# Kernel optimization log

Hardware: AMD Instinct MI355X
Metric: run time of the kernel (lower is better)

The kernel has to match this reference:

```python
import jax, jax.numpy as jnp
import numpy as np

B, C, T, H, W = 2, 256, 16, 32, 32
NH = 8
GROUPS = 32
EPS = 1e-6


def setup_inputs() -> dict:
    key = jax.random.key(0)
    ks = jax.random.split(key, 10)
    r = lambda k, shape: jax.random.normal(k, shape, dtype=jnp.float32) * 0.02
    return dict(
        x=jax.random.normal(ks[0], (B, C, T, H, W), dtype=jnp.float32),
        gn_gamma=jnp.ones((C,), jnp.float32),
        gn_beta=jnp.zeros((C,), jnp.float32),
        wq_s=r(ks[1], (C, C)), bq_s=jnp.zeros((C,), jnp.float32),
        wk_s=r(ks[2], (C, C)), bk_s=jnp.zeros((C,), jnp.float32),
        wv_s=r(ks[3], (C, C)), bv_s=jnp.zeros((C,), jnp.float32),
        wo_s=r(ks[4], (C, C)), bo_s=jnp.zeros((C,), jnp.float32),
        wq_t=r(ks[5], (C, C)),
        wk_t=r(ks[6], (C, C)),
        wv_t=r(ks[7], (C, C)),
        wf_t=r(ks[8], (C, C)), bf_t=jnp.zeros((C,), jnp.float32),
    )


def group_norm(x, gamma, beta):
    # x: (N, C, H, W), GroupNorm(32, eps=1e-6, affine)
    n, c, h, w = x.shape
    xg = x.reshape(n, GROUPS, c // GROUPS, h, w)
    mu = xg.mean(axis=(2, 3, 4), keepdims=True)
    var = xg.var(axis=(2, 3, 4), keepdims=True)
    xg = (xg - mu) * jax.lax.rsqrt(var + EPS)
    return xg.reshape(n, c, h, w) * gamma[None, :, None, None] + beta[None, :, None, None]


def spatial_attention(x, gn_gamma, gn_beta, wq, bq, wk, bk, wv, bv, wo, bo):
    # ldm SpatialSelfAttention: norm -> 1x1 conv q/k/v -> full HW self-attn -> 1x1 proj -> residual
    n, c, h, w = x.shape
    hf = group_norm(x, gn_gamma, gn_beta).reshape(n, c, h * w)  # (N, C, HW)
    q = jnp.einsum('oc,bcn->bno', wq, hf) + bq                  # (N, HW, C)
    k = jnp.einsum('oc,bcn->bon', wk, hf) + bk[None, :, None]   # (N, C, HW)
    v = jnp.einsum('oc,bcn->bon', wv, hf) + bv[None, :, None]   # (N, C, HW)
    attn = jax.nn.softmax(jnp.einsum('bic,bcj->bij', q, k) * (c ** -0.5), axis=-1)  # (N, HW, HW)
    out = jnp.einsum('bcj,bij->bci', v, attn)                   # (N, C, HW)
    out = jnp.einsum('oc,bcn->bon', wo, out) + bo[None, :, None]
    return x + out.reshape(n, c, h, w)


def axial_temporal_attention(x, wq, wk, wv, wf, bf):
    # x: (B, T, H, W, C); VideoGPT MultiHeadAttention with AxialAttention over T (axial_dim=-4)
    b, t, h, w, c = x.shape
    dk = c // NH

    def heads(y):  # (B,T,H,W,C) -> (B,H,W,NH,T,dk)
        return jnp.transpose(y.reshape(b, t, h, w, NH, dk), (0, 2, 3, 4, 1, 5))

    q = heads(x @ wq)
    k = heads(x @ wk)
    v = heads(x @ wv)
    scores = jnp.einsum('bhwntd,bhwnsd->bhwnts', q, k) / jnp.sqrt(jnp.float32(dk))
    attn = jax.nn.softmax(scores, axis=-1)
    out = jnp.einsum('bhwnts,bhwnsd->bhwntd', attn, v)          # (B,H,W,NH,T,dk)
    out = jnp.transpose(out, (0, 4, 1, 2, 3, 5)).reshape(b, t, h, w, c)
    return out @ wf + bf


def reference(x, gn_gamma, gn_beta, wq_s, bq_s, wk_s, bk_s, wv_s, bv_s, wo_s, bo_s,
              wq_t, wk_t, wv_t, wf_t, bf_t):
    b, c, t, h, w = x.shape
    # spatial branch: torch does a raw reshape (B,C,T,H,W)->(B*T,C,H,W); replicate exactly
    s = spatial_attention(x.reshape(b * t, c, h, w), gn_gamma, gn_beta,
                          wq_s, bq_s, wk_s, bk_s, wv_s, bv_s, wo_s, bo_s)
    s = s.reshape(b, c, t, h, w)
    # temporal branch: channels-last, axial attention over T
    xt = jnp.moveaxis(x, 1, -1)                                 # (B,T,H,W,C)
    tt = axial_temporal_attention(xt, wq_t, wk_t, wv_t, wf_t, bf_t)
    return s + jnp.moveaxis(tt, -1, 1)
```

## Files before the change

### kernel.cpp

```cpp
#include <hip/hip_runtime.h>
#include <stdint.h>

typedef uint16_t u16;
typedef __attribute__((ext_vector_type(8))) short s8v;
typedef __attribute__((ext_vector_type(4))) float f32x4;
typedef __attribute__((ext_vector_type(4))) unsigned short us4;

__device__ __forceinline__ float bf2f(u16 u) {
  union { uint32_t i; float f; } x; x.i = ((uint32_t)u) << 16; return x.f;
}
__device__ __forceinline__ u16 f2bf(float f) {
  union { float f; uint32_t i; } x; x.f = f;
  uint32_t r = (x.i + 0x7FFFu + ((x.i >> 16) & 1u)) >> 16;
  return (u16)r;
}
__device__ __forceinline__ void gl2lds16(const u16* g, u16* l) {
  __builtin_amdgcn_global_load_lds(
      (const __attribute__((address_space(1))) uint32_t*)g,
      (__attribute__((address_space(3))) uint32_t*)l, 16, 0, 0);
}

__global__ __launch_bounds__(256) void gn_stats_kernel(const float* __restrict__ x,
                                                       float2* __restrict__ stats) {
  const int tid = threadIdx.x;
  const float* p = x + (long)blockIdx.x * 8192;
  float s = 0.f, s2 = 0.f;
#pragma unroll
  for (int it = 0; it < 8; ++it) {
    float4 v = *(const float4*)(p + it * 1024 + tid * 4);
    s  += v.x + v.y + v.z + v.w;
    s2 += v.x * v.x + v.y * v.y + v.z * v.z + v.w * v.w;
  }
#pragma unroll
  for (int off = 32; off >= 1; off >>= 1) {
    s  += __shfl_down(s, off);
    s2 += __shfl_down(s2, off);
  }
  __shared__ float ps[4], ps2[4];
  const int wv = tid >> 6, lane = tid & 63;
  if (lane == 0) { ps[wv] = s; ps2[wv] = s2; }
  __syncthreads();
  if (tid == 0) {
    float S1 = ps[0] + ps[1] + ps[2] + ps[3];
    float S2 = ps2[0] + ps2[1] + ps2[2] + ps2[3];
    float mean = S1 * (1.f / 8192.f);
    float var = S2 * (1.f / 8192.f) - mean * mean;
    stats[blockIdx.x] = make_float2(mean, rsqrtf(var + 1e-6f));
  }
}

__global__ __launch_bounds__(256) void wprep_kernel(
    const float* __restrict__ s0, const float* __restrict__ s1,
    const float* __restrict__ s2, const float* __restrict__ s3,
    const float* __restrict__ s4, const float* __restrict__ s5,
    const float* __restrict__ s6, const float* __restrict__ s7,
    u16* __restrict__ wbf) {
  const int mat = blockIdx.x, rb = blockIdx.y;
  const float* src = mat==0?s0:mat==1?s1:mat==2?s2:mat==3?s3:mat==4?s4:mat==5?s5:mat==6?s6:s7;
  u16* dst = wbf + mat * 65536 + rb * 16384;
  const int tid = threadIdx.x;
  if (mat < 4) {
    const float* sb = src + rb * 16384;
#pragma unroll
    for (int it = 0; it < 16; ++it) {
      int idx = it * 256 + tid;
      float4 v = *(const float4*)(sb + idx * 4);
      us4 o; o[0]=f2bf(v.x); o[1]=f2bf(v.y); o[2]=f2bf(v.z); o[3]=f2bf(v.w);
      *(us4*)(dst + idx * 4) = o;
    }
  } else {
    __shared__ u16 tl[64][264];
#pragma unroll
    for (int it = 0; it < 16; ++it) {
      int idx = it * 256 + tid;
      int c = idx >> 4, o4 = idx & 15;
      float4 v = *(const float4*)(src + c * 256 + rb * 64 + o4 * 4);
      tl[o4*4+0][c] = f2bf(v.x);
      tl[o4*4+1][c] = f2bf(v.y);
      tl[o4*4+2][c] = f2bf(v.z);
      tl[o4*4+3][c] = f2bf(v.w);
    }
    __syncthreads();
#pragma unroll
    for (int it = 0; it < 16; ++it) {
      int idx = it * 256 + tid;
      int o = idx >> 6, c4 = idx & 63;
      us4 u;
#pragma unroll
      for (int j = 0; j < 4; ++j) u[j] = tl[o][c4*4+j];
      *(us4*)(dst + o * 256 + c4 * 4) = u;
    }
  }
}

__global__ __launch_bounds__(512) void qkv_s_kernel(
    const float* __restrict__ x, const float2* __restrict__ stats,
    const float* __restrict__ gamma, const float* __restrict__ beta,
    const u16* __restrict__ wbf,
    const float* __restrict__ bq, const float* __restrict__ bk, const float* __restrict__ bv,
    u16* __restrict__ qb, u16* __restrict__ kb, u16* __restrict__ vb) {
  __shared__ float gas[256], bes[256];
  __shared__ u16 ALDS[128 * 256];
  __shared__ u16 WLDS[2][64 * 256];
  const int bid = blockIdx.x;
  const int n = bid >> 3, pt = bid & 7;
  const int p0 = pt * 128;
  const int tid = threadIdx.x, w = tid >> 6, lane = tid & 63;
  const int lhi = lane >> 4, llo = lane & 15;
  const long nbase = (long)n * 262144;

  if (tid < 256) {
    float2 st = stats[n * 32 + (tid >> 3)];
    float ga = gamma[tid] * st.y;
    gas[tid] = ga;
    bes[tid] = beta[tid] - st.x * ga;
  }
  __syncthreads();

  const float* xb = x + nbase + p0;
#pragma unroll
  for (int it = 0; it < 16; ++it) {
    int idx = it * 512 + tid;
    int p = idx & 127, c4 = idx >> 7;
    us4 o;
#pragma unroll
    for (int j = 0; j < 4; ++j) {
      int c = c4 * 4 + j;
      float v = xb[(long)c * 1024 + p];
      o[j] = f2bf(v * gas[c] + bes[c]);
    }
    int ch = c4 >> 1;
    *(us4*)&ALDS[p * 256 + ((ch ^ (p & 7)) << 3) + ((c4 & 1) << 2)] = o;
  }
  __syncthreads();

  const int arow = w * 16 + llo;
  s8v qa[8];
#pragma unroll
  for (int kk = 0; kk < 8; ++kk)
    qa[kk] = *(const s8v*)&ALDS[arow * 256 + (((kk * 4 + lhi) ^ (arow & 7)) << 3)];

  auto stageW = [&](int t, int bu) {
    const u16* wsrc = wbf + (t >> 2) * 65536 + (long)(t & 3) * 16384;
#pragma unroll
    for (int ii = 0; ii < 4; ++ii) {
      int i0 = (w * 4 + ii) * 64;
      int g = i0 + lane;
      int row = g >> 5, ch = g & 31;
      gl2lds16(wsrc + row * 256 + ((ch ^ (row & 7)) << 3), &WLDS[bu][i0 * 8]);
    }
  };

  stageW(0, 0);
  __syncthreads();

  u16* vtl = ALDS;
  for (int t = 0; t < 12; ++t) {
    const int cur = t & 1;
    if (t < 11) stageW(t + 1, cur ^ 1);
    f32x4 acc[4] = {};
#pragma unroll
    for (int kk = 0; kk < 8; ++kk)
#pragma unroll
      for (int nf = 0; nf < 4; ++nf) {
        int row = nf * 16 + llo;
        s8v bfr = *(const s8v*)&WLDS[cur][row * 256 + (((kk * 4 + lhi) ^ (row & 7)) << 3)];
        acc[nf] = __builtin_amdgcn_mfma_f32_16x16x32_bf16(qa[kk], bfr, acc[nf], 0, 0, 0);
      }
    const int o0 = (t & 3) * 64;
    if (t < 8) {
      u16* dstb = (t < 4) ? qb : kb;
      const float* bias = (t < 4) ? bq : bk;
#pragma unroll
      for (int nf = 0; nf < 4; ++nf) {
        int o = o0 + nf * 16 + llo;
        float b_ = bias[o];
#pragma unroll
        for (int r = 0; r < 4; ++r)
          dstb[nbase + (long)(p0 + w * 16 + lhi * 4 + r) * 256 + o] = f2bf(acc[nf][r] + b_);
      }
    } else {
#pragma unroll
      for (int nf = 0; nf < 4; ++nf) {
        int o = nf * 16 + llo;
        float b_ = bv[o0 + o];
#pragma unroll
        for (int r = 0; r < 4; ++r)
          vtl[o * 136 + w * 16 + lhi * 4 + r] = f2bf(acc[nf][r] + b_);
      }
      __syncthreads();
#pragma unroll
      for (int ii = 0; ii < 4; ++ii) {
        int i = ii * 512 + tid;
        int o = i >> 5, p4 = (i & 31) * 4;
        us4 u;
#pragma unroll
        for (int j = 0; j < 4; ++j) u[j] = vtl[o * 136 + p4 + j];
        *(us4*)(vb + nbase + (long)(o0 + o) * 1024 + p0 + p4) = u;
      }
    }
    __syncthreads();
  }
}

__global__ __launch_bounds__(512, 2) void flash_kernel(const u16* __restrict__ qb,
                                                       const u16* __restrict__ kb,
                                                       const u16* __restrict__ vb,
                                                       u16* __restrict__ attb) {
  const int wg = blockIdx.x;
  const int swz = (wg & 7) * 32 + (wg >> 3);
  const int n = swz >> 3, qt = swz & 7;
  const int tid = threadIdx.x, wid = tid >> 6, lane = tid & 63;
  const int lhi = lane >> 4, llo = lane & 15;
  const long nbase = (long)n * 262144;

  __shared__ u16 Kb[2][64 * 256];
  __shared__ u16 Vb[2][256 * 64];
  __shared__ u16 ps[128][72];

  const u16* qrow = qb + nbase + (long)(qt * 128 + wid * 16 + llo) * 256;
  s8v qa[8];
#pragma unroll
  for (int kk = 0; kk < 8; ++kk) qa[kk] = *(const s8v*)(qrow + kk * 32 + lhi * 8);

  f32x4 oacc[16] = {};
  float m_[4], l_[4];
#pragma unroll
  for (int r = 0; r < 4; ++r) { m_[r] = -3.4e38f; l_[r] = 0.f; }

  const int l5 = lane >> 5, c16 = lane & 31, l3 = lane >> 3, ch8 = lane & 7;

  auto stageKV = [&](int jt2, int b) {
    const u16* kbase = kb + nbase + (long)jt2 * 64 * 256;
    const u16* vbase = vb + nbase + (long)jt2 * 64;
#pragma unroll
    for (int ii = 0; ii < 4; ++ii) {
      int i = wid * 4 + ii;
      int r = i * 2 + l5;
      gl2lds16(kbase + (long)r * 256 + ((c16 ^ (r & 7)) * 8), &Kb[b][i * 512]);
    }
#pragma unroll
    for (int ii = 0; ii < 4; ++ii) {
      int i = wid * 4 + ii;
      int c = i * 8 + l3;
      gl2lds16(vbase + (long)c * 1024 + ((ch8 ^ (c & 7)) * 8), &Vb[b][i * 512]);
    }
  };

  stageKV(0, 0);
  __syncthreads();

  for (int jt = 0; jt < 16; ++jt) {
    const int cur = jt & 1;
    if (jt < 15) stageKV(jt + 1, cur ^ 1);

    f32x4 sacc[4] = {};
#pragma unroll
    for (int jf = 0; jf < 4; ++jf) {
      const int row = jf * 16 + llo;
      const u16* kr = &Kb[cur][row * 256];
#pragma unroll
      for (int kk = 0; kk < 8; ++kk) {
        const int chunk = (kk * 4 + lhi) ^ (row & 7);
        s8v b = *(const s8v*)(kr + chunk * 8);
        sacc[jf] = __builtin_amdgcn_mfma_f32_16x16x32_bf16(qa[kk], b, sacc[jf], 0, 0, 0);
      }
    }
#pragma unroll
    for (int jf = 0; jf < 4; ++jf)
#pragma unroll
      for (int r = 0; r < 4; ++r) sacc[jf][r] *= 0.0625f;
    float sc[4];
#pragma unroll
    for (int r = 0; r < 4; ++r) {
      float mx = fmaxf(fmaxf(sacc[0][r], sacc[1][r]), fmaxf(sacc[2][r], sacc[3][r]));
      mx = fmaxf(mx, __shfl_xor(mx, 1));
      mx = fmaxf(mx, __shfl_xor(mx, 2));
      mx = fmaxf(mx, __shfl_xor(mx, 4));
      mx = fmaxf(mx, __shfl_xor(mx, 8));
      float nm = fmaxf(m_[r], mx);
      sc[r] = __expf(m_[r] - nm);
      m_[r] = nm;
    }
    float rs[4] = {0.f, 0.f, 0.f, 0.f};
#pragma unroll
    for (int jf = 0; jf < 4; ++jf)
#pragma unroll
      for (int r = 0; r < 4; ++r) {
        float p = __expf(sacc[jf][r] - m_[r]);
        rs[r] += p;
        ps[wid * 16 + lhi * 4 + r][jf * 16 + llo] = f2bf(p);
      }
#pragma unroll
    for (int r = 0; r < 4; ++r) {
      rs[r] += __shfl_xor(rs[r], 1);
      rs[r] += __shfl_xor(rs[r], 2);
      rs[r] += __shfl_xor(rs[r], 4);
      rs[r] += __shfl_xor(rs[r], 8);
      l_[r] = l_[r] * sc[r] + rs[r];
    }
#pragma unroll
    for (int cf = 0; cf < 16; ++cf)
#pragma unroll
      for (int r = 0; r < 4; ++r) oacc[cf][r] *= sc[r];
    s8v pa[2];
#pragma unroll
    for (int kk = 0; kk < 2; ++kk)
      pa[kk] = *(const s8v*)&ps[wid * 16 + llo][kk * 32 + lhi * 8];
#pragma unroll
    for (int cf = 0; cf < 16; ++cf) {
      const int c = cf * 16 + llo;
      const u16* vr = &Vb[cur][c * 64];
#pragma unroll
      for (int kk = 0; kk < 2; ++kk) {
        const int chunk = (kk * 4 + lhi) ^ (c & 7);
        s8v b = *(const s8v*)(vr + chunk * 8);
        oacc[cf] = __builtin_amdgcn_mfma_f32_16x16x32_bf16(pa[kk], b, oacc[cf], 0, 0, 0);
      }
    }
    __syncthreads();
  }
  u16* obase = attb + nbase + (long)(qt * 128 + wid * 16) * 256;
#pragma unroll
  for (int r = 0; r < 4; ++r) {
    float inv = 1.f / l_[r];
#pragma unroll
    for (int cf = 0; cf < 16; ++cf)
      obase[(lhi * 4 + r) * 256 + cf * 16 + llo] = f2bf(oacc[cf][r] * inv);
  }
}

__global__ __launch_bounds__(512) void qkv_t_kernel(
    const float* __restrict__ x, const u16* __restrict__ wbf,
    u16* __restrict__ qt, u16* __restrict__ kt, u16* __restrict__ vt) {
  __shared__ u16 ALDS[128 * 256];
  __shared__ u16 WLDS[2][64 * 256];
  const int bid = blockIdx.x;
  const int b = bid >> 7, st = bid & 127;
  const int s0 = st * 128;
  const int tid = threadIdx.x, w = tid >> 6, lane = tid & 63;
  const int lhi = lane >> 4, llo = lane & 15;
  const long bbase = (long)b * 4194304;

  const float* xb = x + bbase + s0;
#pragma unroll
  for (int it = 0; it < 16; ++it) {
    int idx = it * 512 + tid;
    int p = idx & 127, c4 = idx >> 7;
    us4 o;
#pragma unroll
    for (int j = 0; j < 4; ++j)
      o[j] = f2bf(xb[(long)(c4 * 4 + j) * 16384 + p]);
    int ch = c4 >> 1;
    *(us4*)&ALDS[p * 256 + ((ch ^ (p & 7)) << 3) + ((c4 & 1) << 2)] = o;
  }
  __syncthreads();
  const int arow = w * 16 + llo;
  s8v qa[8];
#pragma unroll
  for (int kk = 0; kk < 8; ++kk)
    qa[kk] = *(const s8v*)&ALDS[arow * 256 + (((kk * 4 + lhi) ^ (arow & 7)) << 3)];

  auto stageW = [&](int t, int bu) {
    const u16* wsrc = wbf + (4 + (t >> 2)) * 65536 + (long)(t & 3) * 16384;
#pragma unroll
    for (int ii = 0; ii < 4; ++ii) {
      int i0 = (w * 4 + ii) * 64;
      int g = i0 + lane;
      int row = g >> 5, ch = g & 31;
      gl2lds16(wsrc + row * 256 + ((ch ^ (row & 7)) << 3), &WLDS[bu][i0 * 8]);
    }
  };
  stageW(0, 0);
  __syncthreads();
  for (int t = 0; t < 12; ++t) {
    const int cur = t & 1;
    if (t < 11) stageW(t + 1, cur ^ 1);
    f32x4 acc[4] = {};
#pragma unroll
    for (int kk = 0; kk < 8; ++kk)
#pragma unroll
      for (int nf = 0; nf < 4; ++nf) {
        int row = nf * 16 + llo;
        s8v bb = *(const s8v*)&WLDS[cur][row * 256 + (((kk * 4 + lhi) ^ (row & 7)) << 3)];
        acc[nf] = __builtin_amdgcn_mfma_f32_16x16x32_bf16(qa[kk], bb, acc[nf], 0, 0, 0);
      }
    u16* dstb = (t < 4) ? qt : (t < 8) ? kt : vt;
    const int o0 = (t & 3) * 64;
#pragma unroll
    for (int nf = 0; nf < 4; ++nf) {
      int o = o0 + nf * 16 + llo;
#pragma unroll
      for (int r = 0; r < 4; ++r)
        dstb[bbase + (long)(s0 + w * 16 + lhi * 4 + r) * 256 + o] = f2bf(acc[nf][r]);
    }
    __syncthreads();
  }
}

__global__ __launch_bounds__(256) void tattn_kernel(const u16* __restrict__ qt,
                                                    const u16* __restrict__ kt,
                                                    const u16* __restrict__ vt,
                                                    u16* __restrict__ ot) {
  const int bi = blockIdx.x >> 10, hw = blockIdx.x & 1023;
  const long base = (long)bi * 4194304 + (long)hw * 256;
  __shared__ float qs[16][260], ks[16][260], vs[16][260];
  __shared__ u16 os[16][256];
  const int tid = threadIdx.x;
#pragma unroll
  for (int it = 0; it < 4; ++it) {
    int idx = it * 256 + tid;
    int t = idx >> 6, cv = idx & 63;
    long g = base + (long)t * 262144 + cv * 4;
    us4 a = *(const us4*)(qt + g);
    us4 b = *(const us4*)(kt + g);
    us4 c = *(const us4*)(vt + g);
#pragma unroll
    for (int j = 0; j < 4; ++j) {
      qs[t][cv * 4 + j] = bf2f(a[j]);
      ks[t][cv * 4 + j] = bf2f(b[j]);
      vs[t][cv * 4 + j] = bf2f(c[j]);
    }
  }
  __syncthreads();
  if (tid < 128) {
    const int h = tid >> 4, t = tid & 15;
    const int c0 = h * 32;
    float sc[16];
    float mx = -3.4e38f;
#pragma unroll
    for (int t2 = 0; t2 < 16; ++t2) {
      float d = 0.f;
#pragma unroll
      for (int dd = 0; dd < 32; ++dd) d += qs[t][c0 + dd] * ks[t2][c0 + dd];
      sc[t2] = d * 0.17677669529663687f;
      mx = fmaxf(mx, sc[t2]);
    }
    float sum = 0.f;
#pragma unroll
    for (int t2 = 0; t2 < 16; ++t2) { sc[t2] = __expf(sc[t2] - mx); sum += sc[t2]; }
    float inv = 1.f / sum;
#pragma unroll
    for (int dd = 0; dd < 32; ++dd) {
      float o = 0.f;
#pragma unroll
      for (int t2 = 0; t2 < 16; ++t2) o += sc[t2] * vs[t2][c0 + dd];
      os[t][c0 + dd] = f2bf(o * inv);
    }
  }
  __syncthreads();
#pragma unroll
  for (int it = 0; it < 4; ++it) {
    int idx = it * 256 + tid;
    int t = idx >> 6, cv = idx & 63;
    us4 o4;
#pragma unroll
    for (int j = 0; j < 4; ++j) o4[j] = os[t][cv * 4 + j];
    *(us4*)(ot + base + (long)t * 262144 + cv * 4) = o4;
  }
}

__global__ __launch_bounds__(512) void tfinal_kernel(
    const u16* __restrict__ ott, const u16* __restrict__ wbf,
    u16* __restrict__ tmpT) {
  __shared__ u16 ALDS[128 * 256];
  __shared__ u16 WLDS[2][64 * 256];
  const int bid = blockIdx.x;
  const int b = bid >> 7, st = bid & 127;
  const int s0 = st * 128;
  const int tid = threadIdx.x, w = tid >> 6, lane = tid & 63;
  const int lhi = lane >> 4, llo = lane & 15;
  const long bbase = (long)b * 4194304;

  const u16* otS = ott + bbase + (long)s0 * 256;
#pragma unroll
  for (int ii = 0; ii < 8; ++ii) {
    int i0 = (w * 8 + ii) * 64;
    int g = i0 + lane;
    int row = g >> 5, ch = g & 31;
    gl2lds16(otS + row * 256 + ((ch ^ (row & 7)) << 3), &ALDS[i0 * 8]);
  }
  __syncthreads();
  const int arow = w * 16 + llo;
  s8v qa[8];
#pragma unroll
  for (int kk = 0; kk < 8; ++kk)
    qa[kk] = *(const s8v*)&ALDS[arow * 256 + (((kk * 4 + lhi) ^ (arow & 7)) << 3)];

  auto stageW = [&](int t, int bu) {
    const u16* wsrc = wbf + 7 * 65536 + (long)t * 16384;
#pragma unroll
    for (int ii = 0; ii < 4; ++ii) {
      int i0 = (w * 4 + ii) * 64;
      int g = i0 + lane;
      int row = g >> 5, ch = g & 31;
      gl2lds16(wsrc + row * 256 + ((ch ^ (row & 7)) << 3), &WLDS[bu][i0 * 8]);
    }
  };
  stageW(0, 0);
  __syncthreads();
  u16* vtl = ALDS;
  for (int t = 0; t < 4; ++t) {
    const int cur = t & 1;
    if (t < 3) stageW(t + 1, cur ^ 1);
    f32x4 acc[4] = {};
#pragma unroll
    for (int kk = 0; kk < 8; ++kk)
#pragma unroll
      for (int nf = 0; nf < 4; ++nf) {
        int row = nf * 16 + llo;
        s8v bb = *(const s8v*)&WLDS[cur][row * 256 + (((kk * 4 + lhi) ^ (row & 7)) << 3)];
        acc[nf] = __builtin_amdgcn_mfma_f32_16x16x32_bf16(qa[kk], bb, acc[nf], 0, 0, 0);
      }
#pragma unroll
    for (int nf = 0; nf < 4; ++nf) {
      int o = nf * 16 + llo;
#pragma unroll
      for (int r = 0; r < 4; ++r)
        vtl[o * 136 + w * 16 + lhi * 4 + r] = f2bf(acc[nf][r]);
    }
    __syncthreads();
    const int o0 = t * 64;
#pragma unroll
    for (int ii = 0; ii < 4; ++ii) {
      int i = ii * 512 + tid;
      int o = i >> 5, p4 = (i & 31) * 4;
      us4 uu;
#pragma unroll
      for (int j = 0; j < 4; ++j) uu[j] = vtl[o * 136 + p4 + j];
      *(us4*)(tmpT + bbase + (long)(o0 + o) * 16384 + s0 + p4) = uu;
    }
    __syncthreads();
  }
}

__global__ __launch_bounds__(256) void outproj_kernel(
    const float* __restrict__ x, const u16* __restrict__ attb,
    const u16* __restrict__ tmpT, const u16* __restrict__ wbf,
    const float* __restrict__ bo, const float* __restrict__ bf,
    float* __restrict__ out) {
  __shared__ u16 attL[64 * 256];
  const int u = blockIdx.x;
  const int wkx = (u & 7) * 256 + (u >> 3);
  const int otile = wkx & 3, pt = (wkx >> 2) & 15, n = wkx >> 6;
  const int b = n >> 4;
  const int o0 = otile * 64, p0 = pt * 64;
  const int tid = threadIdx.x, w = tid >> 6, lane = tid & 63;
  const int lhi = lane >> 4, llo = lane & 15;
  const long nbase = (long)n * 262144;

  const u16* attS = attb + nbase + (long)p0 * 256;
#pragma unroll
  for (int ii = 0; ii < 8; ++ii) {
    int i0 = (w * 8 + ii) * 64;
    int g = i0 + lane;
    int row = g >> 5, ch = g & 31;
    gl2lds16(attS + row * 256 + ((ch ^ (row & 7)) << 3), &attL[i0 * 8]);
  }
  const u16* woR = wbf + 3 * 65536 + (long)(o0 + w * 16 + llo) * 256;
  s8v woa[8];
#pragma unroll
  for (int kk = 0; kk < 8; ++kk)
    woa[kk] = *(const s8v*)(woR + kk * 32 + lhi * 8);
  __syncthreads();
  f32x4 acc[4] = {};
#pragma unroll
  for (int kk = 0; kk < 8; ++kk)
#pragma unroll
    for (int nf = 0; nf < 4; ++nf) {
      int row = nf * 16 + llo;
      s8v b1 = *(const s8v*)&attL[row * 256 + (((kk * 4 + lhi) ^ (row & 7)) << 3)];
      acc[nf] = __builtin_amdgcn_mfma_f32_16x16x32_bf16(woa[kk], b1, acc[nf], 0, 0, 0);
    }
#pragma unroll
  for (int r = 0; r < 4; ++r) {
    int cp = o0 + w * 16 + lhi * 4 + r;
    int co = ((n & 15) << 4) + (cp >> 4);
    int tt = cp & 15;
    float bias = bo[cp] + bf[co];
    const u16* tr = tmpT + (long)b * 4194304 + (long)co * 16384 + tt * 1024 + p0;
    const float* xr = x + nbase + (long)cp * 1024 + p0;
    float* orow = out + nbase + (long)cp * 1024 + p0;
#pragma unroll
    for (int nf = 0; nf < 4; ++nf) {
      int p = nf * 16 + llo;
      orow[p] = acc[nf][r] + bias + xr[p] + bf2f(tr[p]);
    }
  }
}

extern "C" void kernel_launch(void* const* d_in, const int* in_sizes, int n_in,
                              void* d_out, int out_size, void* d_ws, size_t ws_size,
                              hipStream_t stream) {
  const float* x     = (const float*)d_in[0];
  const float* gam   = (const float*)d_in[1];
  const float* bet   = (const float*)d_in[2];
  const float* wq_s  = (const float*)d_in[3];
  const float* bq_s  = (const float*)d_in[4];
  const float* wk_s  = (const float*)d_in[5];
  const float* bk_s  = (const float*)d_in[6];
  const float* wv_s  = (const float*)d_in[7];
  const float* bv_s  = (const float*)d_in[8];
  const float* wo_s  = (const float*)d_in[9];
  const float* bo_s  = (const float*)d_in[10];
  const float* wq_t  = (const float*)d_in[11];
  const float* wk_t  = (const float*)d_in[12];
  const float* wv_t  = (const float*)d_in[13];
  const float* wf_t  = (const float*)d_in[14];
  const float* bf_t  = (const float*)d_in[15];
  float* out = (float*)d_out;

  u16* qb   = (u16*)d_ws;
  u16* kb   = qb + 8388608;
  u16* vb   = kb + 8388608;
  u16* attb = vb + 8388608;
  u16* ottb = attb + 8388608;
  u16* wbf  = ottb + 8388608;
  float2* stats = (float2*)(wbf + 524288);
  u16* qt = qb; u16* kt = kb; u16* vt = vb;
  u16* tmpT = qb;

  gn_stats_kernel<<<1024, 256, 0, stream>>>(x, stats);
  wprep_kernel<<<dim3(8, 4), 256, 0, stream>>>(wq_s, wk_s, wv_s, wo_s,
                                               wq_t, wk_t, wv_t, wf_t, wbf);
  qkv_s_kernel<<<256, 512, 0, stream>>>(x, stats, gam, bet, wbf,
                                        bq_s, bk_s, bv_s, qb, kb, vb);
  flash_kernel<<<256, 512, 0, stream>>>(qb, kb, vb, attb);
  qkv_t_kernel<<<256, 512, 0, stream>>>(x, wbf, qt, kt, vt);
  tattn_kernel<<<2048, 256, 0, stream>>>(qt, kt, vt, ottb);
  tfinal_kernel<<<256, 512, 0, stream>>>(ottb, wbf, tmpT);
  outproj_kernel<<<2048, 256, 0, stream>>>(x, attb, tmpT, wbf, bo_s, bf_t, out);
}
```

Before: 207.2 us.

## Rewrite spatial flash attention with 32x32 MFMA and register-resident P

Measured after the change: 203.0 us. 2.0% less time.

```diff
diff --git a/kernel.cpp b/kernel.cpp
--- a/kernel.cpp
+++ b/kernel.cpp
@@ -4,7 +4,9 @@
 typedef uint16_t u16;
 typedef __attribute__((ext_vector_type(8))) short s8v;
 typedef __attribute__((ext_vector_type(4))) float f32x4;
+typedef __attribute__((ext_vector_type(16))) float f32x16;
 typedef __attribute__((ext_vector_type(4))) unsigned short us4;
+typedef __attribute__((ext_vector_type(4))) unsigned int u32x4;
 
 __device__ __forceinline__ float bf2f(u16 u) {
   union { uint32_t i; float f; } x; x.i = ((uint32_t)u) << 16; return x.f;
@@ -13,6 +15,11 @@
   union { float f; uint32_t i; } x; x.f = f;
   uint32_t r = (x.i + 0x7FFFu + ((x.i >> 16) & 1u)) >> 16;
   return (u16)r;
+}
+__device__ __forceinline__ uint32_t cvtpk(float a, float b) {
+  uint32_t r;
+  asm("v_cvt_pk_bf16_f32 %0, %1, %2" : "=v"(r) : "v"(a), "v"(b));
+  return r;
 }
 __device__ __forceinline__ void gl2lds16(const u16* g, u16* l) {
   __builtin_amdgcn_global_load_lds(
@@ -203,47 +210,44 @@
   }
 }
 
-__global__ __launch_bounds__(512, 2) void flash_kernel(const u16* __restrict__ qb,
+__global__ __launch_bounds__(256, 1) void flash_kernel(const u16* __restrict__ qb,
                                                        const u16* __restrict__ kb,
                                                        const u16* __restrict__ vb,
                                                        u16* __restrict__ attb) {
   const int wg = blockIdx.x;
   const int swz = (wg & 7) * 32 + (wg >> 3);
   const int n = swz >> 3, qt = swz & 7;
-  const int tid = threadIdx.x, wid = tid >> 6, lane = tid & 63;
-  const int lhi = lane >> 4, llo = lane & 15;
+  const int tid = threadIdx.x, w = tid >> 6, lane = tid & 63;
+  const int q5 = lane & 31, h = lane >> 5;
   const long nbase = (long)n * 262144;
 
   __shared__ u16 Kb[2][64 * 256];
   __shared__ u16 Vb[2][256 * 64];
-  __shared__ u16 ps[128][72];
-
-  const u16* qrow = qb + nbase + (long)(qt * 128 + wid * 16 + llo) * 256;
-  s8v qa[8];
-#pragma unroll
-  for (int kk = 0; kk < 8; ++kk) qa[kk] = *(const s8v*)(qrow + kk * 32 + lhi * 8);
-
-  f32x4 oacc[16] = {};
-  float m_[4], l_[4];
-#pragma unroll
-  for (int r = 0; r < 4; ++r) { m_[r] = -3.4e38f; l_[r] = 0.f; }
-
-  const int l5 = lane >> 5, c16 = lane & 31, l3 = lane >> 3, ch8 = lane & 7;
+
+  const int qrow = qt * 128 + w * 32 + q5;
+  const u16* qr = qb + nbase + (long)qrow * 256 + h * 8;
+  s8v qa[16];
+#pragma unroll
+  for (int kk = 0; kk < 16; ++kk) qa[kk] = *(const s8v*)(qr + kk * 16);
+
+  f32x16 oaccT[8] = {};
+  float m_ = -3.4e38f, l_ = 0.f;
+  constexpr float CEXP = 0.09016844f;
 
   auto stageKV = [&](int jt2, int b) {
     const u16* kbase = kb + nbase + (long)jt2 * 64 * 256;
     const u16* vbase = vb + nbase + (long)jt2 * 64;
 #pragma unroll
-    for (int ii = 0; ii < 4; ++ii) {
-      int i = wid * 4 + ii;
-      int r = i * 2 + l5;
-      gl2lds16(kbase + (long)r * 256 + ((c16 ^ (r & 7)) * 8), &Kb[b][i * 512]);
-    }
-#pragma unroll
-    for (int ii = 0; ii < 4; ++ii) {
-      int i = wid * 4 + ii;
-      int c = i * 8 + l3;
-      gl2lds16(vbase + (long)c * 1024 + ((ch8 ^ (c & 7)) * 8), &Vb[b][i * 512]);
+    for (int ii = 0; ii < 8; ++ii) {
+      int slot = ii * 256 + tid;
+      int row = slot >> 5, ch = slot & 31;
+      gl2lds16(kbase + (long)row * 256 + ((ch ^ (row & 7)) << 3), &Kb[b][slot * 8]);
+    }
+#pragma unroll
+    for (int ii = 0; ii < 8; ++ii) {
+      int slot = ii * 256 + tid;
+      int c = slot >> 3, ch = slot & 7;
+      gl2lds16(vbase + (long)c * 1024 + ((ch ^ (c & 7)) << 3), &Vb[b][slot * 8]);
     }
   };
 
@@ -254,79 +258,96 @@
     const int cur = jt & 1;
     if (jt < 15) stageKV(jt + 1, cur ^ 1);
 
-    f32x4 sacc[4] = {};
-#pragma unroll
-    for (int jf = 0; jf < 4; ++jf) {
-      const int row = jf * 16 + llo;
-      const u16* kr = &Kb[cur][row * 256];
-#pragma unroll
-      for (int kk = 0; kk < 8; ++kk) {
-        const int chunk = (kk * 4 + lhi) ^ (row & 7);
-        s8v b = *(const s8v*)(kr + chunk * 8);
-        sacc[jf] = __builtin_amdgcn_mfma_f32_16x16x32_bf16(qa[kk], b, sacc[jf], 0, 0, 0);
-      }
-    }
-#pragma unroll
-    for (int jf = 0; jf < 4; ++jf)
-#pragma unroll
-      for (int r = 0; r < 4; ++r) sacc[jf][r] *= 0.0625f;
-    float sc[4];
-#pragma unroll
-    for (int r = 0; r < 4; ++r) {
-      float mx = fmaxf(fmaxf(sacc[0][r], sacc[1][r]), fmaxf(sacc[2][r], sacc[3][r]));
-      mx = fmaxf(mx, __shfl_xor(mx, 1));
-      mx = fmaxf(mx, __shfl_xor(mx, 2));
-      mx = fmaxf(mx, __shfl_xor(mx, 4));
-      mx = fmaxf(mx, __shfl_xor(mx, 8));
-      float nm = fmaxf(m_[r], mx);
-      sc[r] = __expf(m_[r] - nm);
-      m_[r] = nm;
-    }
-    float rs[4] = {0.f, 0.f, 0.f, 0.f};
-#pragma unroll
-    for (int jf = 0; jf < 4; ++jf)
-#pragma unroll
-      for (int r = 0; r < 4; ++r) {
-        float p = __expf(sacc[jf][r] - m_[r]);
-        rs[r] += p;
-        ps[wid * 16 + lhi * 4 + r][jf * 16 + llo] = f2bf(p);
-      }
-#pragma unroll
-    for (int r = 0; r < 4; ++r) {
-      rs[r] += __shfl_xor(rs[r], 1);
-      rs[r] += __shfl_xor(rs[r], 2);
-      rs[r] += __shfl_xor(rs[r], 4);
-      rs[r] += __shfl_xor(rs[r], 8);
-      l_[r] = l_[r] * sc[r] + rs[r];
-    }
-#pragma unroll
-    for (int cf = 0; cf < 16; ++cf)
-#pragma unroll
-      for (int r = 0; r < 4; ++r) oacc[cf][r] *= sc[r];
-    s8v pa[2];
-#pragma unroll
-    for (int kk = 0; kk < 2; ++kk)
-      pa[kk] = *(const s8v*)&ps[wid * 16 + llo][kk * 32 + lhi * 8];
-#pragma unroll
-    for (int cf = 0; cf < 16; ++cf) {
-      const int c = cf * 16 + llo;
-      const u16* vr = &Vb[cur][c * 64];
-#pragma unroll
-      for (int kk = 0; kk < 2; ++kk) {
-        const int chunk = (kk * 4 + lhi) ^ (c & 7);
-        s8v b = *(const s8v*)(vr + chunk * 8);
-        oacc[cf] = __builtin_amdgcn_mfma_f32_16x16x32_bf16(pa[kk], b, oacc[cf], 0, 0, 0);
+    f32x16 sacc[2] = {};
+#pragma unroll
+    for (int kk = 0; kk < 16; ++kk) {
+#pragma unroll
+      for (int f = 0; f < 2; ++f) {
+        int krow = f * 32 + q5;
+        s8v kfr = *(const s8v*)&Kb[cur][krow * 256 + (((kk * 2 + h) ^ (q5 & 7)) << 3)];
+        sacc[f] = __builtin_amdgcn_mfma_f32_32x32x16_bf16(kfr, qa[kk], sacc[f], 0, 0, 0);
+      }
+    }
+    float pm = sacc[0][0];
+#pragma unroll
+    for (int f = 0; f < 2; ++f)
+#pragma unroll
+      for (int r = 0; r < 16; ++r) pm = fmaxf(pm, sacc[f][r]);
+    pm = fmaxf(pm, __shfl_xor(pm, 32));
+    if (!__all(pm <= m_ + 128.f)) {
+      float scf = exp2f((m_ - pm) * CEXP);
+      l_ *= scf;
+#pragma unroll
+      for (int cf = 0; cf < 8; ++cf)
+#pragma unroll
+        for (int r = 0; r < 16; ++r) oaccT[cf][r] *= scf;
+      m_ = pm;
+    }
+    float rs = 0.f;
+#pragma unroll
+    for (int f = 0; f < 2; ++f)
+#pragma unroll
+      for (int r = 0; r < 16; ++r) {
+        float p = exp2f((sacc[f][r] - m_) * CEXP);
+        sacc[f][r] = p;
+        rs += p;
+      }
+    rs += __shfl_xor(rs, 32);
+    l_ += rs;
+    uint32_t pk[2][4][2];
+#pragma unroll
+    for (int f = 0; f < 2; ++f)
+#pragma unroll
+      for (int g = 0; g < 4; ++g) {
+        pk[f][g][0] = cvtpk(sacc[f][4 * g + 0], sacc[f][4 * g + 1]);
+        pk[f][g][1] = cvtpk(sacc[f][4 * g + 2], sacc[f][4 * g + 3]);
+      }
+#pragma unroll
+    for (int js = 0; js < 4; ++js) {
+      const int f = js >> 1, g0 = 2 * (js & 1);
+      uint32_t own0 = h ? pk[f][g0 + 1][0] : pk[f][g0][0];
+      uint32_t own1 = h ? pk[f][g0 + 1][1] : pk[f][g0][1];
+      uint32_t snd0 = h ? pk[f][g0][0] : pk[f][g0 + 1][0];
+      uint32_t snd1 = h ? pk[f][g0][1] : pk[f][g0 + 1][1];
+      uint32_t rcv0 = __shfl_xor(snd0, 32);
+      uint32_t rcv1 = __shfl_xor(snd1, 32);
+      u32x4 pw;
+      pw[0] = h ? rcv0 : own0;
+      pw[1] = h ? rcv1 : own1;
+      pw[2] = h ? own0 : rcv0;
+      pw[3] = h ? own1 : rcv1;
+      s8v pa = __builtin_bit_cast(s8v, pw);
+#pragma unroll
+      for (int cf = 0; cf < 8; ++cf) {
+        int c = cf * 32 + q5;
+        s8v vfr = *(const s8v*)&Vb[cur][c * 64 + (((js * 2 + h) ^ (q5 & 7)) << 3)];
+        oaccT[cf] = __builtin_amdgcn_mfma_f32_32x32x16_bf16(vfr, pa, oaccT[cf], 0, 0, 0);
       }
     }
     __syncthreads();
   }
-  u16* obase = attb + nbase + (long)(qt * 128 + wid * 16) * 256;
-#pragma unroll
-  for (int r = 0; r < 4; ++r) {
-    float inv = 1.f / l_[r];
-#pragma unroll
-    for (int cf = 0; cf < 16; ++cf)
-      obase[(lhi * 4 + r) * 256 + cf * 16 + llo] = f2bf(oacc[cf][r] * inv);
+  float inv = 1.f / l_;
+  u16* tl = &Kb[0][0];
+  __syncthreads();
+  const int myq = w * 32 + q5;
+#pragma unroll
+  for (int cf = 0; cf < 8; ++cf)
+#pragma unroll
+    for (int g = 0; g < 4; ++g) {
+      uint32_t w0 = cvtpk(oaccT[cf][4 * g + 0] * inv, oaccT[cf][4 * g + 1] * inv);
+      uint32_t w1 = cvtpk(oaccT[cf][4 * g + 2] * inv, oaccT[cf][4 * g + 3] * inv);
+      int ch = (cf * 4 + g) ^ (myq & 7);
+      uint2 val; val.x = w0; val.y = w1;
+      *(uint2*)&tl[myq * 256 + ch * 8 + h * 4] = val;
+    }
+  __syncthreads();
+  const int qo = tid >> 1, hr = tid & 1;
+  u16* obase = attb + nbase + (long)(qt * 128 + qo) * 256;
+#pragma unroll
+  for (int u = 0; u < 16; ++u) {
+    int c16 = hr * 16 + u;
+    u32x4 v = *(const u32x4*)&tl[qo * 256 + ((c16 ^ (qo & 7)) << 3)];
+    *(u32x4*)(obase + c16 * 8) = v;
   }
 }
 
@@ -625,7 +646,7 @@
                                                wq_t, wk_t, wv_t, wf_t, wbf);
   qkv_s_kernel<<<256, 512, 0, stream>>>(x, stats, gam, bet, wbf,
                                         bq_s, bk_s, bv_s, qb, kb, vb);
-  flash_kernel<<<256, 512, 0, stream>>>(qb, kb, vb, attb);
+  flash_kernel<<<256, 256, 0, stream>>>(qb, kb, vb, attb);
   qkv_t_kernel<<<256, 512, 0, stream>>>(x, wbf, qt, kt, vt);
   tattn_kernel<<<2048, 256, 0, stream>>>(qt, kt, vt, ottb);
   tfinal_kernel<<<256, 512, 0, stream>>>(ottb, wbf, tmpT);
```
